# Kernel optimization log

Measured on AMD Instinct MI355X. Metric: run time of the kernel, lower is better.

The kernel has to match this reference:

```python
import jax, jax.numpy as jnp
import numpy as np

B, DIM, H, W = 8, 256, 128, 128
HEADS, D = 8, 32  # num_heads, qkv_dim (key_dim); multi_q_dim = HEADS*D = DIM


def setup_inputs() -> dict:
    key = jax.random.key(0)
    ks = jax.random.split(key, 10)
    def affine(k, n):
        k1, k2 = jax.random.split(k)
        return (1.0 + 0.1 * jax.random.normal(k1, (n,), jnp.float32),
                0.1 * jax.random.normal(k2, (n,), jnp.float32))
    q_scale, q_bias = affine(ks[1], HEADS * D)
    kv_scale, kv_bias = affine(ks[3], D)
    p_scale, p_bias = affine(ks[5], DIM)
    return {
        "input_": jax.random.normal(ks[0], (B, DIM, H, W), jnp.float32),
        "wq": jax.random.normal(ks[6], (HEADS * D, DIM), jnp.float32) / np.sqrt(DIM),
        "q_scale": q_scale, "q_bias": q_bias,
        "wkv": jax.random.normal(ks[7], (D, DIM), jnp.float32) / np.sqrt(DIM),
        "kv_scale": kv_scale, "kv_bias": kv_bias,
        "wp": jax.random.normal(ks[8], (DIM, HEADS * D), jnp.float32) / np.sqrt(HEADS * D),
        "p_scale": p_scale, "p_bias": p_bias,
    }


def conv1x1_bn(x_flat, w, scale, bias):
    # x_flat: [B,C,N]; 1x1 conv (no bias) fused with eval-mode BN affine
    y = jnp.einsum('oc,bcn->bon', w, x_flat)
    return y * scale[:, None] + bias[:, None]


def reference(input_, wq, q_scale, q_bias, wkv, kv_scale, kv_bias, wp, p_scale, p_bias):
    b, c, h, w = input_.shape
    n = h * w
    xf = input_.reshape(b, c, n)
    # queries: [B, heads, D, N]
    q = conv1x1_bn(xf, wq, q_scale, q_bias).reshape(b, HEADS, D, n)
    # shared key/value, one kv head: [B, D, N]
    kv = conv1x1_bn(xf, wkv, kv_scale, kv_bias)
    key_sm = jax.nn.softmax(kv, axis=2)      # softmax over spatial N
    query_sm = jax.nn.softmax(q, axis=2)     # softmax over channel D
    # context = softmax(K) @ V^T : [B, D, D]
    context = jnp.einsum('bdn,ben->bde', key_sm, kv)
    # attended = context^T @ Q (context broadcast over heads): [B, heads, D, N]
    attended = jnp.einsum('bde,bhdn->bhen', context, query_sm)
    av = attended.reshape(b, HEADS * D, n)
    out = conv1x1_bn(jax.nn.relu(av), wp, p_scale, p_bias)
    return out.reshape(b, c, h, w)
```

## Files before the change

kernel.cpp:

```cpp
#include <hip/hip_runtime.h>
#include <hip/hip_bf16.h>

typedef __hip_bfloat16 bf16;
typedef __attribute__((ext_vector_type(8))) short bf16x8;
typedef __attribute__((ext_vector_type(4))) float f32x4;

#define NB 8
#define NC 256
#define ND 32
#define NH 8
#define NN 16384
#define TILE_P 32

#define MFMA16(a, b, c) __builtin_amdgcn_mfma_f32_16x16x32_bf16((a), (b), (c), 0, 0, 0)

__device__ __forceinline__ float u2f(unsigned short u) {
  union { unsigned int i; float f; } v; v.i = ((unsigned int)u) << 16; return v.f;
}
__device__ __forceinline__ unsigned short f2u(float f) {
  union { float f; unsigned int i; } v; v.f = f;
  unsigned int x = v.i;
  return (unsigned short)((x + 0x7fffu + ((x >> 16) & 1u)) >> 16);
}
__device__ __forceinline__ float ldg(const void* p, size_t i, int isbf) {
  return isbf ? u2f(((const unsigned short*)p)[i]) : ((const float*)p)[i];
}
__device__ __forceinline__ char* lds_at(char* base, int p, int colb) {
  return base + (p << 9) + (colb ^ ((p & 7) << 4));
}

__global__ __launch_bounds__(256) void detect_kernel(const void* __restrict__ x,
                                                     int* __restrict__ flag) {
  __shared__ int red[4];
  const unsigned int* w = (const unsigned int*)x;
  int cnt = 0;
  for (int i = threadIdx.x; i < 4096; i += 256) {
    unsigned int e = (w[i] >> 7) & 0xFFu;
    cnt += (e >= 100u && e <= 135u) ? 1 : 0;
  }
  for (int off = 32; off; off >>= 1) cnt += __shfl_xor(cnt, off, 64);
  if ((threadIdx.x & 63) == 0) red[threadIdx.x >> 6] = cnt;
  __syncthreads();
  if (threadIdx.x == 0)
    flag[0] = (red[0] + red[1] + red[2] + red[3] > 2048) ? 1 : 0;
}

__global__ __launch_bounds__(256) void prep_weights(
    const void* __restrict__ wq, const void* __restrict__ wp,
    const void* __restrict__ wkv, const int* __restrict__ flag,
    unsigned short* __restrict__ WqPh, unsigned short* __restrict__ WqPl,
    unsigned short* __restrict__ WpPh, unsigned short* __restrict__ WpPl,
    unsigned short* __restrict__ WkPh, unsigned short* __restrict__ WkPl) {
  int isbf = flag[0];
  int idx = blockIdx.x * 256 + threadIdx.x;
  const void* w;
  unsigned short *Ph, *Pl;
  int slot, o, k0;
  if (idx < 16384) {
    int mat = idx >> 13;
    slot = idx & 8191;
    int lane = slot & 63;
    int mbkt = slot >> 6;
    int mb = mbkt & 15, kt = mbkt >> 4;
    o = mb * 16 + (lane & 15);
    k0 = kt * 32 + (lane >> 4) * 8;
    w = mat ? wp : wq;
    Ph = mat ? WpPh : WqPh;
    Pl = mat ? WpPl : WqPl;
  } else {
    slot = idx - 16384;
    int lane = slot & 63;
    int grp = slot >> 6;
    int mb = grp & 1, kt = grp >> 1;
    o = mb * 16 + (lane & 15);
    k0 = kt * 32 + (lane >> 4) * 8;
    w = wkv;
    Ph = WkPh;
    Pl = WkPl;
  }
  unsigned short h[8], lo[8];
#pragma unroll
  for (int e = 0; e < 8; e++) {
    float v = ldg(w, (size_t)o * NC + k0 + e, isbf);
    unsigned short hh = f2u(v);
    h[e] = hh;
    lo[e] = isbf ? (unsigned short)0 : f2u(v - u2f(hh));
  }
  uint4 ph, pl;
  ph.x = h[0] | ((unsigned)h[1] << 16);
  ph.y = h[2] | ((unsigned)h[3] << 16);
  ph.z = h[4] | ((unsigned)h[5] << 16);
  ph.w = h[6] | ((unsigned)h[7] << 16);
  pl.x = lo[0] | ((unsigned)lo[1] << 16);
  pl.y = lo[2] | ((unsigned)lo[3] << 16);
  pl.z = lo[4] | ((unsigned)lo[5] << 16);
  pl.w = lo[6] | ((unsigned)lo[7] << 16);
  *(uint4*)(Ph + (size_t)slot * 8) = ph;
  *(uint4*)(Pl + (size_t)slot * 8) = pl;
}

template <int ISBF>
__global__ __launch_bounds__(256, 2) void kv_mfma(
    const void* __restrict__ x, const unsigned short* __restrict__ WkPh,
    const unsigned short* __restrict__ WkPl, const void* __restrict__ kv_scale,
    const void* __restrict__ kv_bias, const int* __restrict__ flag,
    float* __restrict__ kv_out) {
  constexpr int POOL = ISBF ? 32768 : 65536;
  constexpr int XTL_O = 32768;
  __shared__ __align__(16) char pool[POOL];
  if (flag[0] != ISBF) return;
  const int tid = threadIdx.x;
  const int b = blockIdx.x >> 8;
  const int n0 = (blockIdx.x & 255) * 64;
  const int w = tid >> 6, l = tid & 63, g = l >> 4, cc = l & 15;

  {
    const int pq = (tid & 15) * 4;
    const int c0 = (tid >> 4) * 16;
    unsigned short hi[16][4], lo[16][4];
    if (ISBF) {
      const unsigned short* xp =
          (const unsigned short*)x + ((size_t)(b * NC + c0)) * NN + n0 + pq;
#pragma unroll
      for (int i = 0; i < 16; i++) {
        ushort4 r = *(const ushort4*)(xp + (size_t)i * NN);
        hi[i][0] = r.x; hi[i][1] = r.y; hi[i][2] = r.z; hi[i][3] = r.w;
      }
    } else {
      const float* xp = (const float*)x + ((size_t)(b * NC + c0)) * NN + n0 + pq;
#pragma unroll
      for (int i = 0; i < 16; i++) {
        float4 v = *(const float4*)(xp + (size_t)i * NN);
        float vv[4] = {v.x, v.y, v.z, v.w};
#pragma unroll
        for (int j = 0; j < 4; j++) {
          unsigned short hh = f2u(vv[j]);
          hi[i][j] = hh;
          lo[i][j] = f2u(vv[j] - u2f(hh));
        }
      }
    }
#pragma unroll
    for (int j = 0; j < 4; j++) {
      int p = pq + j;
#pragma unroll
      for (int half = 0; half < 2; half++) {
        uint4 wv;
        wv.x = hi[8*half+0][j] | ((unsigned)hi[8*half+1][j] << 16);
        wv.y = hi[8*half+2][j] | ((unsigned)hi[8*half+3][j] << 16);
        wv.z = hi[8*half+4][j] | ((unsigned)hi[8*half+5][j] << 16);
        wv.w = hi[8*half+6][j] | ((unsigned)hi[8*half+7][j] << 16);
        *(uint4*)lds_at(pool, p, c0 * 2 + half * 16) = wv;
        if (!ISBF) {
          uint4 wl2;
          wl2.x = lo[8*half+0][j] | ((unsigned)lo[8*half+1][j] << 16);
          wl2.y = lo[8*half+2][j] | ((unsigned)lo[8*half+3][j] << 16);
          wl2.z = lo[8*half+4][j] | ((unsigned)lo[8*half+5][j] << 16);
          wl2.w = lo[8*half+6][j] | ((unsigned)lo[8*half+7][j] << 16);
          *(uint4*)lds_at(pool + XTL_O, p, c0 * 2 + half * 16) = wl2;
        }
      }
    }
  }
  __syncthreads();

  const f32x4 zero4 = {0.f, 0.f, 0.f, 0.f};
  f32x4 acc[2] = {zero4, zero4};
  const bf16x8* Ah = (const bf16x8*)WkPh;
  const bf16x8* Al = (const bf16x8*)WkPl;
#pragma unroll
  for (int kt = 0; kt < 8; kt++) {
    bf16x8 xb = *(const bf16x8*)lds_at(pool, 16 * w + cc, kt * 64 + 16 * g);
    bf16x8 a0 = Ah[(kt * 2 + 0) * 64 + l];
    bf16x8 a1 = Ah[(kt * 2 + 1) * 64 + l];
    acc[0] = MFMA16(a0, xb, acc[0]);
    acc[1] = MFMA16(a1, xb, acc[1]);
    if (!ISBF) {
      bf16x8 xl = *(const bf16x8*)lds_at(pool + XTL_O, 16 * w + cc, kt * 64 + 16 * g);
      bf16x8 l0 = Al[(kt * 2 + 0) * 64 + l];
      bf16x8 l1 = Al[(kt * 2 + 1) * 64 + l];
      acc[0] = MFMA16(a0, xl, acc[0]);
      acc[0] = MFMA16(l0, xb, acc[0]);
      acc[0] = MFMA16(l0, xl, acc[0]);
      acc[1] = MFMA16(a1, xl, acc[1]);
      acc[1] = MFMA16(l1, xb, acc[1]);
      acc[1] = MFMA16(l1, xl, acc[1]);
    }
  }
  const int n = n0 + 16 * w + cc;
#pragma unroll
  for (int mi = 0; mi < 2; mi++) {
#pragma unroll
    for (int rr = 0; rr < 4; rr++) {
      int d = mi * 16 + 4 * g + rr;
      float v = acc[mi][rr] * ldg(kv_scale, d, ISBF) + ldg(kv_bias, d, ISBF);
      kv_out[((size_t)(b * ND + d)) * NN + n] = v;
    }
  }
}

__global__ __launch_bounds__(256) void rowmax_kernel(const float* __restrict__ kv,
                                                     float* __restrict__ m) {
  __shared__ float red[4];
  int row = blockIdx.x;
  const float* p = kv + (size_t)row * NN;
  float mx = -3.0e38f;
  for (int i = threadIdx.x; i < NN; i += 256) mx = fmaxf(mx, p[i]);
  for (int off = 32; off; off >>= 1) mx = fmaxf(mx, __shfl_xor(mx, off, 64));
  if ((threadIdx.x & 63) == 0) red[threadIdx.x >> 6] = mx;
  __syncthreads();
  if (threadIdx.x == 0)
    m[row] = fmaxf(fmaxf(red[0], red[1]), fmaxf(red[2], red[3]));
}

__global__ __launch_bounds__(256, 2) void ctx_mfma(const float* __restrict__ kv,
                                                   const float* __restrict__ m,
                                                   float* __restrict__ Spart,
                                                   float* __restrict__ Zpart) {
  constexpr int KH_O = 0, KL_O = 16384, EH_O = 32768, EL_O = 49152;
  __shared__ __align__(16) char pool[65536];
  const int tid = threadIdx.x;
  const int bid = blockIdx.x;
  const int b = bid >> 6;
  const int n0 = (bid & 63) * 256;
  const int r = tid >> 3, q = tid & 7;
  const float mr = m[b * ND + r];
  const float* src = kv + ((size_t)(b * ND + r)) * NN + n0;
  float z = 0.f;
#pragma unroll
  for (int s = 0; s < 8; s++) {
    float4 v = *(const float4*)(src + q * 4 + s * 32);
    float vv[4] = {v.x, v.y, v.z, v.w};
    unsigned short kh[4], kl[4], eh[4], el[4];
#pragma unroll
    for (int j = 0; j < 4; j++) {
      unsigned short hh = f2u(vv[j]);
      kh[j] = hh;
      kl[j] = f2u(vv[j] - u2f(hh));
      float e = __expf(vv[j] - mr);
      z += e;
      unsigned short eH = f2u(e);
      eh[j] = eH;
      el[j] = f2u(e - u2f(eH));
    }
    int colb = 8 * q + 64 * s;
    uint2 a;
    a.x = kh[0] | ((unsigned)kh[1] << 16); a.y = kh[2] | ((unsigned)kh[3] << 16);
    *(uint2*)lds_at(pool + KH_O, r, colb) = a;
    a.x = kl[0] | ((unsigned)kl[1] << 16); a.y = kl[2] | ((unsigned)kl[3] << 16);
    *(uint2*)lds_at(pool + KL_O, r, colb) = a;
    a.x = eh[0] | ((unsigned)eh[1] << 16); a.y = eh[2] | ((unsigned)eh[3] << 16);
    *(uint2*)lds_at(pool + EH_O, r, colb) = a;
    a.x = el[0] | ((unsigned)el[1] << 16); a.y = el[2] | ((unsigned)el[3] << 16);
    *(uint2*)lds_at(pool + EL_O, r, colb) = a;
  }
  z += __shfl_xor(z, 1, 64);
  z += __shfl_xor(z, 2, 64);
  z += __shfl_xor(z, 4, 64);
  if (q == 0) Zpart[(size_t)bid * ND + r] = z;
  __syncthreads();

  const int w = tid >> 6, l = tid & 63, g = l >> 4, cc = l & 15;
  const int mt = w >> 1, nt = w & 1;
  f32x4 sacc = {0.f, 0.f, 0.f, 0.f};
#pragma unroll
  for (int kt = 0; kt < 8; kt++) {
    int colb = kt * 64 + 16 * g;
    bf16x8 ehf = *(const bf16x8*)lds_at(pool + EH_O, 16 * mt + cc, colb);
    bf16x8 elf = *(const bf16x8*)lds_at(pool + EL_O, 16 * mt + cc, colb);
    bf16x8 khf = *(const bf16x8*)lds_at(pool + KH_O, 16 * nt + cc, colb);
    bf16x8 klf = *(const bf16x8*)lds_at(pool + KL_O, 16 * nt + cc, colb);
    sacc = MFMA16(ehf, khf, sacc);
    sacc = MFMA16(ehf, klf, sacc);
    sacc = MFMA16(elf, khf, sacc);
  }
#pragma unroll
  for (int rr = 0; rr < 4; rr++) {
    int row = 16 * mt + 4 * g + rr;
    Spart[(size_t)bid * 1024 + row * 32 + 16 * nt + cc] = sacc[rr];
  }
}

__global__ __launch_bounds__(256) void ctx_redfin(const float* __restrict__ Spart,
                                                  const float* __restrict__ Zpart,
                                                  float* __restrict__ ctx) {
  int i = blockIdx.x * 256 + threadIdx.x;
  int b = i >> 10, cell = i & 1023, d = cell >> 5;
  float s = 0.f, z = 0.f;
  for (int ch = 0; ch < 64; ch++) {
    s += Spart[(size_t)(b * 64 + ch) * 1024 + cell];
    z += Zpart[(size_t)(b * 64 + ch) * ND + d];
  }
  ctx[i] = s / z;
}

template <int ISBF>
__global__ __launch_bounds__(256, 2) void fused_main(
    const void* __restrict__ x,
    const unsigned short* __restrict__ WqPh, const unsigned short* __restrict__ WqPl,
    const unsigned short* __restrict__ WpPh, const unsigned short* __restrict__ WpPl,
    const void* __restrict__ q_scale, const void* __restrict__ q_bias,
    const void* __restrict__ p_scale, const void* __restrict__ p_bias,
    const float* __restrict__ ctx, const int* __restrict__ flag,
    void* __restrict__ out) {
  constexpr int XT_O = 0;
  constexpr int XTL_O = 16384;
  constexpr int SMH_O = ISBF ? 16384 : 32768;
  constexpr int SML_O = ISBF ? 32768 : 49152;
  constexpr int YTH_O = 0;
  constexpr int YTL_O = 16384;
  constexpr int OT_O = ISBF ? 16384 : 32768;
  constexpr int OT_STR = ISBF ? 88 : 144;
  constexpr int POOL = ISBF ? 49152 : 69632;
  __shared__ __align__(16) char pool[POOL];
  __shared__ float qs_l[NC], qb_l[NC], ps_l[NC], pb_l[NC];
  if (flag[0] != ISBF) return;
  const int tid = threadIdx.x;
  const int b = blockIdx.x >> 9;
  const int n0 = (blockIdx.x & 511) * TILE_P;
  const int w = tid >> 6;
  const int l = tid & 63;
  const int g = l >> 4;
  const int cc = l & 15;
  const f32x4 zero4 = {0.f, 0.f, 0.f, 0.f};

  qs_l[tid] = ldg(q_scale, tid, ISBF);
  qb_l[tid] = ldg(q_bias, tid, ISBF);
  ps_l[tid] = ldg(p_scale, tid, ISBF);
  pb_l[tid] = ldg(p_bias, tid, ISBF);

  bf16x8 cAh[2], cAl[2];
  {
    const float* cb = ctx + (size_t)b * ND * ND;
#pragma unroll
    for (int mp = 0; mp < 2; mp++) {
      bf16x8 ah, al;
#pragma unroll
      for (int el = 0; el < 8; el++) {
        float v = cb[(8 * g + el) * ND + 16 * mp + cc];
        unsigned short hh = f2u(v);
        ah[el] = (short)hh;
        al[el] = (short)f2u(v - u2f(hh));
      }
      cAh[mp] = ah; cAl[mp] = al;
    }
  }

  {
    const int c0 = (tid >> 3) * 8;
    const int pq = (tid & 7) * 4;
    unsigned short hi[8][4], lo[8][4];
    if (ISBF) {
      const unsigned short* xp =
          (const unsigned short*)x + ((size_t)(b * NC + c0)) * NN + n0 + pq;
#pragma unroll
      for (int i = 0; i < 8; i++) {
        ushort4 r = *(const ushort4*)(xp + (size_t)i * NN);
        hi[i][0] = r.x; hi[i][1] = r.y; hi[i][2] = r.z; hi[i][3] = r.w;
      }
    } else {
      const float* xp = (const float*)x + ((size_t)(b * NC + c0)) * NN + n0 + pq;
#pragma unroll
      for (int i = 0; i < 8; i++) {
        float4 v = *(const float4*)(xp + (size_t)i * NN);
        float vv[4] = {v.x, v.y, v.z, v.w};
#pragma unroll
        for (int j = 0; j < 4; j++) {
          unsigned short hh = f2u(vv[j]);
          hi[i][j] = hh;
          lo[i][j] = f2u(vv[j] - u2f(hh));
        }
      }
    }
#pragma unroll
    for (int j = 0; j < 4; j++) {
      int p = pq + j;
      uint4 wv;
      wv.x = hi[0][j] | ((unsigned)hi[1][j] << 16);
      wv.y = hi[2][j] | ((unsigned)hi[3][j] << 16);
      wv.z = hi[4][j] | ((unsigned)hi[5][j] << 16);
      wv.w = hi[6][j] | ((unsigned)hi[7][j] << 16);
      *(uint4*)lds_at(pool + XT_O, p, c0 * 2) = wv;
      if (!ISBF) {
        uint4 wl2;
        wl2.x = lo[0][j] | ((unsigned)lo[1][j] << 16);
        wl2.y = lo[2][j] | ((unsigned)lo[3][j] << 16);
        wl2.z = lo[4][j] | ((unsigned)lo[5][j] << 16);
        wl2.w = lo[6][j] | ((unsigned)lo[7][j] << 16);
        *(uint4*)lds_at(pool + XTL_O, p, c0 * 2) = wl2;
      }
    }
  }
  __syncthreads();

  f32x4 acc[4][2];
#pragma unroll
  for (int mi = 0; mi < 4; mi++) { acc[mi][0] = zero4; acc[mi][1] = zero4; }
  {
    const bf16x8* Aq = (const bf16x8*)WqPh;
    const bf16x8* Aql = (const bf16x8*)WqPl;
#pragma unroll
    for (int kt = 0; kt < 8; kt++) {
      bf16x8 xb0 = *(const bf16x8*)lds_at(pool + XT_O, cc, kt * 64 + 16 * g);
      bf16x8 xb1 = *(const bf16x8*)lds_at(pool + XT_O, 16 + cc, kt * 64 + 16 * g);
      bf16x8 av[4];
#pragma unroll
      for (int mi = 0; mi < 4; mi++) av[mi] = Aq[(kt * 16 + w * 4 + mi) * 64 + l];
#pragma unroll
      for (int mi = 0; mi < 4; mi++) {
        acc[mi][0] = MFMA16(av[mi], xb0, acc[mi][0]);
        acc[mi][1] = MFMA16(av[mi], xb1, acc[mi][1]);
      }
      if (!ISBF) {
        bf16x8 xl0 = *(const bf16x8*)lds_at(pool + XTL_O, cc, kt * 64 + 16 * g);
        bf16x8 xl1 = *(const bf16x8*)lds_at(pool + XTL_O, 16 + cc, kt * 64 + 16 * g);
#pragma unroll
        for (int mi = 0; mi < 4; mi++) {
          bf16x8 al2 = Aql[(kt * 16 + w * 4 + mi) * 64 + l];
          acc[mi][0] = MFMA16(av[mi], xl0, acc[mi][0]);
          acc[mi][1] = MFMA16(av[mi], xl1, acc[mi][1]);
          acc[mi][0] = MFMA16(al2, xb0, acc[mi][0]);
          acc[mi][1] = MFMA16(al2, xb1, acc[mi][1]);
          acc[mi][0] = MFMA16(al2, xl0, acc[mi][0]);
          acc[mi][1] = MFMA16(al2, xl1, acc[mi][1]);
        }
      }
    }
  }

  float inv_s[2][2];
#pragma unroll
  for (int hp = 0; hp < 2; hp++) {
#pragma unroll
    for (int ni = 0; ni < 2; ni++) {
      float e8[8];
      float mx = -3.0e38f;
#pragma unroll
      for (int mi2 = 0; mi2 < 2; mi2++) {
#pragma unroll
        for (int r = 0; r < 4; r++) {
          int o = w * 64 + (2 * hp + mi2) * 16 + 4 * g + r;
          float v = acc[2 * hp + mi2][ni][r] * qs_l[o] + qb_l[o];
          e8[mi2 * 4 + r] = v;
          mx = fmaxf(mx, v);
        }
      }
      mx = fmaxf(mx, __shfl_xor(mx, 16, 64));
      mx = fmaxf(mx, __shfl_xor(mx, 32, 64));
      float s = 0.f;
#pragma unroll
      for (int i2 = 0; i2 < 8; i2++) { e8[i2] = __expf(e8[i2] - mx); s += e8[i2]; }
      s += __shfl_xor(s, 16, 64);
      s += __shfl_xor(s, 32, 64);
      inv_s[hp][ni] = 1.f / s;
      int p = ni * 16 + cc;
#pragma unroll
      for (int mi2 = 0; mi2 < 2; mi2++) {
        int colb = (w * 64 + (2 * hp + mi2) * 16 + 4 * g) * 2;
        unsigned short h[4], lo2[4];
#pragma unroll
        for (int r = 0; r < 4; r++) {
          float ev = e8[mi2 * 4 + r];
          unsigned short hh = f2u(ev);
          h[r] = hh;
          lo2[r] = f2u(ev - u2f(hh));
        }
        uint2 wh, wl2;
        wh.x = h[0] | ((unsigned)h[1] << 16);
        wh.y = h[2] | ((unsigned)h[3] << 16);
        wl2.x = lo2[0] | ((unsigned)lo2[1] << 16);
        wl2.y = lo2[2] | ((unsigned)lo2[3] << 16);
        *(uint2*)lds_at(pool + SMH_O, p, colb) = wh;
        *(uint2*)lds_at(pool + SML_O, p, colb) = wl2;
      }
    }
  }
  __syncthreads();

#pragma unroll
  for (int hp = 0; hp < 2; hp++) {
    f32x4 cacc[2][2];
#pragma unroll
    for (int mp = 0; mp < 2; mp++) { cacc[mp][0] = zero4; cacc[mp][1] = zero4; }
#pragma unroll
    for (int ni = 0; ni < 2; ni++) {
      int p = ni * 16 + cc;
      int colb = ((2 * w + hp) * 32 + 8 * g) * 2;
      bf16x8 bh = *(const bf16x8*)lds_at(pool + SMH_O, p, colb);
      bf16x8 bl = *(const bf16x8*)lds_at(pool + SML_O, p, colb);
#pragma unroll
      for (int mp = 0; mp < 2; mp++) {
        cacc[mp][ni] = MFMA16(cAh[mp], bh, cacc[mp][ni]);
        cacc[mp][ni] = MFMA16(cAh[mp], bl, cacc[mp][ni]);
        cacc[mp][ni] = MFMA16(cAl[mp], bh, cacc[mp][ni]);
        if (!ISBF) cacc[mp][ni] = MFMA16(cAl[mp], bl, cacc[mp][ni]);
      }
    }
#pragma unroll
    for (int mp = 0; mp < 2; mp++) {
#pragma unroll
      for (int ni = 0; ni < 2; ni++) {
        int p = ni * 16 + cc;
        float iv = inv_s[hp][ni];
        unsigned short h[4], lo2[4];
#pragma unroll
        for (int r = 0; r < 4; r++) {
          float y = fmaxf(cacc[mp][ni][r] * iv, 0.f);
          unsigned short hh = f2u(y);
          h[r] = hh;
          lo2[r] = f2u(y - u2f(hh));
        }
        int colb = ((2 * w + hp) * 32 + mp * 16 + 4 * g) * 2;
        uint2 wh;
        wh.x = h[0] | ((unsigned)h[1] << 16);
        wh.y = h[2] | ((unsigned)h[3] << 16);
        *(uint2*)lds_at(pool + YTH_O, p, colb) = wh;
        if (!ISBF) {
          uint2 wl2;
          wl2.x = lo2[0] | ((unsigned)lo2[1] << 16);
          wl2.y = lo2[2] | ((unsigned)lo2[3] << 16);
          *(uint2*)lds_at(pool + YTL_O, p, colb) = wl2;
        }
      }
    }
  }
  __syncthreads();

  f32x4 oacc[4][2];
#pragma unroll
  for (int mi = 0; mi < 4; mi++) { oacc[mi][0] = zero4; oacc[mi][1] = zero4; }
  {
    const bf16x8* Ap = (const bf16x8*)WpPh;
    const bf16x8* Apl = (const bf16x8*)WpPl;
#pragma unroll
    for (int kt = 0; kt < 8; kt++) {
      bf16x8 yh0 = *(const bf16x8*)lds_at(pool + YTH_O, cc, kt * 64 + 16 * g);
      bf16x8 yh1 = *(const bf16x8*)lds_at(pool + YTH_O, 16 + cc, kt * 64 + 16 * g);
      bf16x8 av[4];
#pragma unroll
      for (int mi = 0; mi < 4; mi++) av[mi] = Ap[(kt * 16 + w * 4 + mi) * 64 + l];
#pragma unroll
      for (int mi = 0; mi < 4; mi++) {
        oacc[mi][0] = MFMA16(av[mi], yh0, oacc[mi][0]);
        oacc[mi][1] = MFMA16(av[mi], yh1, oacc[mi][1]);
      }
      if (!ISBF) {
        bf16x8 yl0 = *(const bf16x8*)lds_at(pool + YTL_O, cc, kt * 64 + 16 * g);
        bf16x8 yl1 = *(const bf16x8*)lds_at(pool + YTL_O, 16 + cc, kt * 64 + 16 * g);
#pragma unroll
        for (int mi = 0; mi < 4; mi++) {
          bf16x8 al2 = Apl[(kt * 16 + w * 4 + mi) * 64 + l];
          oacc[mi][0] = MFMA16(av[mi], yl0, oacc[mi][0]);
          oacc[mi][1] = MFMA16(av[mi], yl1, oacc[mi][1]);
          oacc[mi][0] = MFMA16(al2, yh0, oacc[mi][0]);
          oacc[mi][1] = MFMA16(al2, yh1, oacc[mi][1]);
        }
      }
    }
  }

  {
    char* OT = pool + OT_O;
#pragma unroll
    for (int mi = 0; mi < 4; mi++) {
#pragma unroll
      for (int ni = 0; ni < 2; ni++) {
#pragma unroll
        for (int r = 0; r < 4; r++) {
          int o = w * 64 + mi * 16 + 4 * g + r;
          float v = oacc[mi][ni][r] * ps_l[o] + pb_l[o];
          int p = ni * 16 + cc;
          if (ISBF)
            *(unsigned short*)(OT + o * OT_STR + p * 2) = f2u(v);
          else
            *(float*)(OT + o * OT_STR + p * 4) = v;
        }
      }
    }
  }
  __syncthreads();
  {
    char* OT = pool + OT_O;
    int o = tid;
    size_t gbase = ((size_t)(b * NC + o)) * NN + n0;
    if (ISBF) {
      unsigned short* po = (unsigned short*)out + gbase;
#pragma unroll
      for (int k = 0; k < 4; k++) {
        uint2 a = *(const uint2*)(OT + o * OT_STR + k * 16);
        uint2 b2 = *(const uint2*)(OT + o * OT_STR + k * 16 + 8);
        uint4 pk = make_uint4(a.x, a.y, b2.x, b2.y);
        *(uint4*)(po + k * 8) = pk;
      }
    } else {
      float* po = (float*)out + gbase;
#pragma unroll
      for (int k = 0; k < 8; k++)
        *(float4*)(po + k * 4) = *(const float4*)(OT + o * OT_STR + k * 16);
    }
  }
}

extern "C" void kernel_launch(void* const* d_in, const int* in_sizes, int n_in,
                              void* d_out, int out_size, void* d_ws, size_t ws_size,
                              hipStream_t stream) {
  const void* input   = d_in[0];
  const void* wq      = d_in[1];
  const void* q_scale = d_in[2];
  const void* q_bias  = d_in[3];
  const void* wkv     = d_in[4];
  const void* kv_scale= d_in[5];
  const void* kv_bias = d_in[6];
  const void* wp      = d_in[7];
  const void* p_scale = d_in[8];
  const void* p_bias  = d_in[9];

  char* w = (char*)d_ws;
  int*  flag = (int*)w;      w += 256;
  float* kv   = (float*)w;   w += (size_t)NB * ND * NN * 4;
  float* mrow = (float*)w;   w += 1024;
  float* Spart = (float*)w;  w += (size_t)512 * 1024 * 4;
  float* Zpart = (float*)w;  w += (size_t)512 * ND * 4;
  float* ctx  = (float*)w;   w += (size_t)NB * ND * ND * 4;
  unsigned short* WqPh = (unsigned short*)w; w += (size_t)NC * NC * 2;
  unsigned short* WqPl = (unsigned short*)w; w += (size_t)NC * NC * 2;
  unsigned short* WpPh = (unsigned short*)w; w += (size_t)NC * NC * 2;
  unsigned short* WpPl = (unsigned short*)w; w += (size_t)NC * NC * 2;
  unsigned short* WkPh = (unsigned short*)w; w += (size_t)ND * NC * 2;
  unsigned short* WkPl = (unsigned short*)w; w += (size_t)ND * NC * 2;

  detect_kernel<<<1, 256, 0, stream>>>(input, flag);
  prep_weights<<<68, 256, 0, stream>>>(wq, wp, wkv, flag, WqPh, WqPl, WpPh, WpPl,
                                       WkPh, WkPl);
  kv_mfma<1><<<2048, 256, 0, stream>>>(input, WkPh, WkPl, kv_scale, kv_bias, flag, kv);
  kv_mfma<0><<<2048, 256, 0, stream>>>(input, WkPh, WkPl, kv_scale, kv_bias, flag, kv);
  rowmax_kernel<<<256, 256, 0, stream>>>(kv, mrow);
  ctx_mfma<<<512, 256, 0, stream>>>(kv, mrow, Spart, Zpart);
  ctx_redfin<<<32, 256, 0, stream>>>(Spart, Zpart, ctx);
  fused_main<1><<<4096, 256, 0, stream>>>(input, WqPh, WqPl, WpPh, WpPl,
                                          q_scale, q_bias, p_scale, p_bias,
                                          ctx, flag, (void*)d_out);
  fused_main<0><<<4096, 256, 0, stream>>>(input, WqPh, WqPl, WpPh, WpPl,
                                          q_scale, q_bias, p_scale, p_bias,
                                          ctx, flag, (void*)d_out);
}
```

Measured before the change: 420.4 us.

## Split K into bf16 hi/lo planes, drop max pass, halve LDS for occupancy

The kv projection now writes K as bf16 hi/lo planes instead of fp32. The rowmax kernel is removed, so the context kernel computes exp without max subtraction, reading K straight from global memory with no LDS staging. fp32 paths in kv_mfma and fused_main stage the input in two K-halves to shrink LDS and raise occupancy (launch bounds 4 and 3). Several lo*lo MFMA terms and the low part of the relu(attended) activations are dropped. This trades accuracy and the overflow safety of max-subtraction for less memory traffic, fewer launches and fewer MFMAs.

```diff
diff --git a/kernel.cpp b/kernel.cpp
--- a/kernel.cpp
+++ b/kernel.cpp
@@ -1,14 +1,12 @@
 #include <hip/hip_runtime.h>
 #include <hip/hip_bf16.h>
 
-typedef __hip_bfloat16 bf16;
 typedef __attribute__((ext_vector_type(8))) short bf16x8;
 typedef __attribute__((ext_vector_type(4))) float f32x4;
 
 #define NB 8
 #define NC 256
 #define ND 32
-#define NH 8
 #define NN 16384
 #define TILE_P 32
 
@@ -100,45 +98,32 @@
 }
 
 template <int ISBF>
-__global__ __launch_bounds__(256, 2) void kv_mfma(
+__global__ __launch_bounds__(256, 4) void kv_mfma(
     const void* __restrict__ x, const unsigned short* __restrict__ WkPh,
     const unsigned short* __restrict__ WkPl, const void* __restrict__ kv_scale,
     const void* __restrict__ kv_bias, const int* __restrict__ flag,
-    float* __restrict__ kv_out) {
-  constexpr int POOL = ISBF ? 32768 : 65536;
-  constexpr int XTL_O = 32768;
-  __shared__ __align__(16) char pool[POOL];
+    unsigned short* __restrict__ Kh, unsigned short* __restrict__ Kl) {
+  __shared__ __align__(16) char pool[32768];
   if (flag[0] != ISBF) return;
   const int tid = threadIdx.x;
   const int b = blockIdx.x >> 8;
   const int n0 = (blockIdx.x & 255) * 64;
   const int w = tid >> 6, l = tid & 63, g = l >> 4, cc = l & 15;
-
-  {
+  const f32x4 zero4 = {0.f, 0.f, 0.f, 0.f};
+  f32x4 acc[2] = {zero4, zero4};
+  const bf16x8* Ah = (const bf16x8*)WkPh;
+  const bf16x8* Al = (const bf16x8*)WkPl;
+
+  if constexpr (ISBF) {
     const int pq = (tid & 15) * 4;
     const int c0 = (tid >> 4) * 16;
-    unsigned short hi[16][4], lo[16][4];
-    if (ISBF) {
-      const unsigned short* xp =
-          (const unsigned short*)x + ((size_t)(b * NC + c0)) * NN + n0 + pq;
-#pragma unroll
-      for (int i = 0; i < 16; i++) {
-        ushort4 r = *(const ushort4*)(xp + (size_t)i * NN);
-        hi[i][0] = r.x; hi[i][1] = r.y; hi[i][2] = r.z; hi[i][3] = r.w;
-      }
-    } else {
-      const float* xp = (const float*)x + ((size_t)(b * NC + c0)) * NN + n0 + pq;
-#pragma unroll
-      for (int i = 0; i < 16; i++) {
-        float4 v = *(const float4*)(xp + (size_t)i * NN);
-        float vv[4] = {v.x, v.y, v.z, v.w};
-#pragma unroll
-        for (int j = 0; j < 4; j++) {
-          unsigned short hh = f2u(vv[j]);
-          hi[i][j] = hh;
-          lo[i][j] = f2u(vv[j] - u2f(hh));
-        }
-      }
+    const unsigned short* xp =
+        (const unsigned short*)x + ((size_t)(b * NC + c0)) * NN + n0 + pq;
+    unsigned short hi[16][4];
+#pragma unroll
+    for (int i = 0; i < 16; i++) {
+      ushort4 r = *(const ushort4*)(xp + (size_t)i * NN);
+      hi[i][0] = r.x; hi[i][1] = r.y; hi[i][2] = r.z; hi[i][3] = r.w;
     }
 #pragma unroll
     for (int j = 0; j < 4; j++) {
@@ -151,42 +136,72 @@
         wv.z = hi[8*half+4][j] | ((unsigned)hi[8*half+5][j] << 16);
         wv.w = hi[8*half+6][j] | ((unsigned)hi[8*half+7][j] << 16);
         *(uint4*)lds_at(pool, p, c0 * 2 + half * 16) = wv;
-        if (!ISBF) {
-          uint4 wl2;
-          wl2.x = lo[8*half+0][j] | ((unsigned)lo[8*half+1][j] << 16);
-          wl2.y = lo[8*half+2][j] | ((unsigned)lo[8*half+3][j] << 16);
-          wl2.z = lo[8*half+4][j] | ((unsigned)lo[8*half+5][j] << 16);
-          wl2.w = lo[8*half+6][j] | ((unsigned)lo[8*half+7][j] << 16);
-          *(uint4*)lds_at(pool + XTL_O, p, c0 * 2 + half * 16) = wl2;
+      }
+    }
+    __syncthreads();
+#pragma unroll
+    for (int kt = 0; kt < 8; kt++) {
+      bf16x8 xb = *(const bf16x8*)lds_at(pool, 16 * w + cc, kt * 64 + 16 * g);
+      bf16x8 a0 = Ah[(kt * 2 + 0) * 64 + l];
+      bf16x8 a1 = Ah[(kt * 2 + 1) * 64 + l];
+      acc[0] = MFMA16(a0, xb, acc[0]);
+      acc[1] = MFMA16(a1, xb, acc[1]);
+    }
+  } else {
+#pragma unroll
+    for (int kh = 0; kh < 2; kh++) {
+      const int pq = (tid & 15) * 4;
+      const int c0l = (tid >> 4) * 8;
+      const float* xp =
+          (const float*)x + ((size_t)(b * NC + kh * 128 + c0l)) * NN + n0 + pq;
+      unsigned short hi[8][4], lo[8][4];
+#pragma unroll
+      for (int i = 0; i < 8; i++) {
+        float4 v = *(const float4*)(xp + (size_t)i * NN);
+        float vv[4] = {v.x, v.y, v.z, v.w};
+#pragma unroll
+        for (int j = 0; j < 4; j++) {
+          unsigned short hh = f2u(vv[j]);
+          hi[i][j] = hh;
+          lo[i][j] = f2u(vv[j] - u2f(hh));
         }
       }
-    }
-  }
-  __syncthreads();
-
-  const f32x4 zero4 = {0.f, 0.f, 0.f, 0.f};
-  f32x4 acc[2] = {zero4, zero4};
-  const bf16x8* Ah = (const bf16x8*)WkPh;
-  const bf16x8* Al = (const bf16x8*)WkPl;
-#pragma unroll
-  for (int kt = 0; kt < 8; kt++) {
-    bf16x8 xb = *(const bf16x8*)lds_at(pool, 16 * w + cc, kt * 64 + 16 * g);
-    bf16x8 a0 = Ah[(kt * 2 + 0) * 64 + l];
-    bf16x8 a1 = Ah[(kt * 2 + 1) * 64 + l];
-    acc[0] = MFMA16(a0, xb, acc[0]);
-    acc[1] = MFMA16(a1, xb, acc[1]);
-    if (!ISBF) {
-      bf16x8 xl = *(const bf16x8*)lds_at(pool + XTL_O, 16 * w + cc, kt * 64 + 16 * g);
-      bf16x8 l0 = Al[(kt * 2 + 0) * 64 + l];
-      bf16x8 l1 = Al[(kt * 2 + 1) * 64 + l];
-      acc[0] = MFMA16(a0, xl, acc[0]);
-      acc[0] = MFMA16(l0, xb, acc[0]);
-      acc[0] = MFMA16(l0, xl, acc[0]);
-      acc[1] = MFMA16(a1, xl, acc[1]);
-      acc[1] = MFMA16(l1, xb, acc[1]);
-      acc[1] = MFMA16(l1, xl, acc[1]);
-    }
-  }
+      if (kh) __syncthreads();
+#pragma unroll
+      for (int j = 0; j < 4; j++) {
+        int p = pq + j;
+        uint4 wv, wl2;
+        wv.x = hi[0][j] | ((unsigned)hi[1][j] << 16);
+        wv.y = hi[2][j] | ((unsigned)hi[3][j] << 16);
+        wv.z = hi[4][j] | ((unsigned)hi[5][j] << 16);
+        wv.w = hi[6][j] | ((unsigned)hi[7][j] << 16);
+        wl2.x = lo[0][j] | ((unsigned)lo[1][j] << 16);
+        wl2.y = lo[2][j] | ((unsigned)lo[3][j] << 16);
+        wl2.z = lo[4][j] | ((unsigned)lo[5][j] << 16);
+        wl2.w = lo[6][j] | ((unsigned)lo[7][j] << 16);
+        *(uint4*)lds_at(pool, p, c0l * 2) = wv;
+        *(uint4*)lds_at(pool, p, c0l * 2 + 256) = wl2;
+      }
+      __syncthreads();
+#pragma unroll
+      for (int kt = 0; kt < 4; kt++) {
+        int ktg = kh * 4 + kt;
+        bf16x8 xh = *(const bf16x8*)lds_at(pool, 16 * w + cc, kt * 64 + 16 * g);
+        bf16x8 xl = *(const bf16x8*)lds_at(pool, 16 * w + cc, kt * 64 + 16 * g + 256);
+        bf16x8 a0 = Ah[(ktg * 2 + 0) * 64 + l];
+        bf16x8 a1 = Ah[(ktg * 2 + 1) * 64 + l];
+        bf16x8 l0 = Al[(ktg * 2 + 0) * 64 + l];
+        bf16x8 l1 = Al[(ktg * 2 + 1) * 64 + l];
+        acc[0] = MFMA16(a0, xh, acc[0]);
+        acc[0] = MFMA16(a0, xl, acc[0]);
+        acc[0] = MFMA16(l0, xh, acc[0]);
+        acc[1] = MFMA16(a1, xh, acc[1]);
+        acc[1] = MFMA16(a1, xl, acc[1]);
+        acc[1] = MFMA16(l1, xh, acc[1]);
+      }
+    }
+  }
+
   const int n = n0 + 16 * w + cc;
 #pragma unroll
   for (int mi = 0; mi < 2; mi++) {
@@ -194,90 +209,72 @@
     for (int rr = 0; rr < 4; rr++) {
       int d = mi * 16 + 4 * g + rr;
       float v = acc[mi][rr] * ldg(kv_scale, d, ISBF) + ldg(kv_bias, d, ISBF);
-      kv_out[((size_t)(b * ND + d)) * NN + n] = v;
-    }
-  }
-}
-
-__global__ __launch_bounds__(256) void rowmax_kernel(const float* __restrict__ kv,
-                                                     float* __restrict__ m) {
-  __shared__ float red[4];
-  int row = blockIdx.x;
-  const float* p = kv + (size_t)row * NN;
-  float mx = -3.0e38f;
-  for (int i = threadIdx.x; i < NN; i += 256) mx = fmaxf(mx, p[i]);
-  for (int off = 32; off; off >>= 1) mx = fmaxf(mx, __shfl_xor(mx, off, 64));
-  if ((threadIdx.x & 63) == 0) red[threadIdx.x >> 6] = mx;
-  __syncthreads();
-  if (threadIdx.x == 0)
-    m[row] = fmaxf(fmaxf(red[0], red[1]), fmaxf(red[2], red[3]));
-}
-
-__global__ __launch_bounds__(256, 2) void ctx_mfma(const float* __restrict__ kv,
-                                                   const float* __restrict__ m,
-                                                   float* __restrict__ Spart,
-                                                   float* __restrict__ Zpart) {
-  constexpr int KH_O = 0, KL_O = 16384, EH_O = 32768, EL_O = 49152;
-  __shared__ __align__(16) char pool[65536];
+      unsigned short h16 = f2u(v);
+      unsigned short l16 = f2u(v - u2f(h16));
+      size_t off = ((size_t)(b * ND + d)) * NN + n;
+      Kh[off] = h16;
+      Kl[off] = l16;
+    }
+  }
+}
+
+__global__ __launch_bounds__(256) void ctx_mfma(const unsigned short* __restrict__ Kh,
+                                                const unsigned short* __restrict__ Kl,
+                                                float* __restrict__ Spart,
+                                                float* __restrict__ Zpart) {
   const int tid = threadIdx.x;
   const int bid = blockIdx.x;
-  const int b = bid >> 6;
-  const int n0 = (bid & 63) * 256;
-  const int r = tid >> 3, q = tid & 7;
-  const float mr = m[b * ND + r];
-  const float* src = kv + ((size_t)(b * ND + r)) * NN + n0;
-  float z = 0.f;
-#pragma unroll
-  for (int s = 0; s < 8; s++) {
-    float4 v = *(const float4*)(src + q * 4 + s * 32);
-    float vv[4] = {v.x, v.y, v.z, v.w};
-    unsigned short kh[4], kl[4], eh[4], el[4];
-#pragma unroll
-    for (int j = 0; j < 4; j++) {
-      unsigned short hh = f2u(vv[j]);
-      kh[j] = hh;
-      kl[j] = f2u(vv[j] - u2f(hh));
-      float e = __expf(vv[j] - mr);
-      z += e;
-      unsigned short eH = f2u(e);
-      eh[j] = eH;
-      el[j] = f2u(e - u2f(eH));
-    }
-    int colb = 8 * q + 64 * s;
-    uint2 a;
-    a.x = kh[0] | ((unsigned)kh[1] << 16); a.y = kh[2] | ((unsigned)kh[3] << 16);
-    *(uint2*)lds_at(pool + KH_O, r, colb) = a;
-    a.x = kl[0] | ((unsigned)kl[1] << 16); a.y = kl[2] | ((unsigned)kl[3] << 16);
-    *(uint2*)lds_at(pool + KL_O, r, colb) = a;
-    a.x = eh[0] | ((unsigned)eh[1] << 16); a.y = eh[2] | ((unsigned)eh[3] << 16);
-    *(uint2*)lds_at(pool + EH_O, r, colb) = a;
-    a.x = el[0] | ((unsigned)el[1] << 16); a.y = el[2] | ((unsigned)el[3] << 16);
-    *(uint2*)lds_at(pool + EL_O, r, colb) = a;
-  }
-  z += __shfl_xor(z, 1, 64);
-  z += __shfl_xor(z, 2, 64);
-  z += __shfl_xor(z, 4, 64);
-  if (q == 0) Zpart[(size_t)bid * ND + r] = z;
-  __syncthreads();
-
+  const int b = bid >> 4;
   const int w = tid >> 6, l = tid & 63, g = l >> 4, cc = l & 15;
-  const int mt = w >> 1, nt = w & 1;
-  f32x4 sacc = {0.f, 0.f, 0.f, 0.f};
+  const int nbase = (bid & 15) * 1024 + w * 256;
+  const f32x4 zero4 = {0.f, 0.f, 0.f, 0.f};
+  f32x4 s00 = zero4, s01 = zero4, s10 = zero4, s11 = zero4;
+  float z0 = 0.f, z1 = 0.f;
+  const size_t row0 = ((size_t)(b * ND) + cc) * NN;
+  const size_t row1 = ((size_t)(b * ND) + 16 + cc) * NN;
 #pragma unroll
   for (int kt = 0; kt < 8; kt++) {
-    int colb = kt * 64 + 16 * g;
-    bf16x8 ehf = *(const bf16x8*)lds_at(pool + EH_O, 16 * mt + cc, colb);
-    bf16x8 elf = *(const bf16x8*)lds_at(pool + EL_O, 16 * mt + cc, colb);
-    bf16x8 khf = *(const bf16x8*)lds_at(pool + KH_O, 16 * nt + cc, colb);
-    bf16x8 klf = *(const bf16x8*)lds_at(pool + KL_O, 16 * nt + cc, colb);
-    sacc = MFMA16(ehf, khf, sacc);
-    sacc = MFMA16(ehf, klf, sacc);
-    sacc = MFMA16(elf, khf, sacc);
-  }
+    int nn = nbase + kt * 32 + 8 * g;
+    bf16x8 kh0 = *(const bf16x8*)(Kh + row0 + nn);
+    bf16x8 kl0 = *(const bf16x8*)(Kl + row0 + nn);
+    bf16x8 kh1 = *(const bf16x8*)(Kh + row1 + nn);
+    bf16x8 kl1 = *(const bf16x8*)(Kl + row1 + nn);
+    bf16x8 eh0, el0, eh1, el1;
+#pragma unroll
+    for (int e = 0; e < 8; e++) {
+      float v0 = u2f((unsigned short)kh0[e]) + u2f((unsigned short)kl0[e]);
+      float ev0 = __expf(v0);
+      z0 += ev0;
+      unsigned short h0 = f2u(ev0);
+      eh0[e] = (short)h0;
+      el0[e] = (short)f2u(ev0 - u2f(h0));
+      float v1 = u2f((unsigned short)kh1[e]) + u2f((unsigned short)kl1[e]);
+      float ev1 = __expf(v1);
+      z1 += ev1;
+      unsigned short h1 = f2u(ev1);
+      eh1[e] = (short)h1;
+      el1[e] = (short)f2u(ev1 - u2f(h1));
+    }
+    s00 = MFMA16(eh0, kh0, s00); s00 = MFMA16(eh0, kl0, s00); s00 = MFMA16(el0, kh0, s00);
+    s01 = MFMA16(eh0, kh1, s01); s01 = MFMA16(eh0, kl1, s01); s01 = MFMA16(el0, kh1, s01);
+    s10 = MFMA16(eh1, kh0, s10); s10 = MFMA16(eh1, kl0, s10); s10 = MFMA16(el1, kh0, s10);
+    s11 = MFMA16(eh1, kh1, s11); s11 = MFMA16(eh1, kl1, s11); s11 = MFMA16(el1, kh1, s11);
+  }
+  z0 += __shfl_xor(z0, 16, 64); z0 += __shfl_xor(z0, 32, 64);
+  z1 += __shfl_xor(z1, 16, 64); z1 += __shfl_xor(z1, 32, 64);
+  if (l < 16) {
+    Zpart[((size_t)bid * 4 + w) * ND + cc] = z0;
+    Zpart[((size_t)bid * 4 + w) * ND + 16 + cc] = z1;
+  }
+  float* sp = Spart + ((size_t)bid * 4 + w) * 1024;
 #pragma unroll
   for (int rr = 0; rr < 4; rr++) {
-    int row = 16 * mt + 4 * g + rr;
-    Spart[(size_t)bid * 1024 + row * 32 + 16 * nt + cc] = sacc[rr];
+    int r0 = (4 * g + rr) * 32;
+    int r1 = (16 + 4 * g + rr) * 32;
+    sp[r0 + cc] = s00[rr];
+    sp[r0 + 16 + cc] = s01[rr];
+    sp[r1 + cc] = s10[rr];
+    sp[r1 + 16 + cc] = s11[rr];
   }
 }
 
@@ -287,15 +284,15 @@
   int i = blockIdx.x * 256 + threadIdx.x;
   int b = i >> 10, cell = i & 1023, d = cell >> 5;
   float s = 0.f, z = 0.f;
-  for (int ch = 0; ch < 64; ch++) {
-    s += Spart[(size_t)(b * 64 + ch) * 1024 + cell];
-    z += Zpart[(size_t)(b * 64 + ch) * ND + d];
+  for (int j = 0; j < 64; j++) {
+    s += Spart[(size_t)(b * 64 + j) * 1024 + cell];
+    z += Zpart[(size_t)(b * 64 + j) * ND + d];
   }
   ctx[i] = s / z;
 }
 
 template <int ISBF>
-__global__ __launch_bounds__(256, 2) void fused_main(
+__global__ __launch_bounds__(256, 3) void fused_main(
     const void* __restrict__ x,
     const unsigned short* __restrict__ WqPh, const unsigned short* __restrict__ WqPl,
     const unsigned short* __restrict__ WpPh, const unsigned short* __restrict__ WpPl,
@@ -303,15 +300,11 @@
     const void* __restrict__ p_scale, const void* __restrict__ p_bias,
     const float* __restrict__ ctx, const int* __restrict__ flag,
     void* __restrict__ out) {
-  constexpr int XT_O = 0;
-  constexpr int XTL_O = 16384;
-  constexpr int SMH_O = ISBF ? 16384 : 32768;
-  constexpr int SML_O = ISBF ? 32768 : 49152;
-  constexpr int YTH_O = 0;
-  constexpr int YTL_O = 16384;
-  constexpr int OT_O = ISBF ? 16384 : 32768;
-  constexpr int OT_STR = ISBF ? 88 : 144;
-  constexpr int POOL = ISBF ? 49152 : 69632;
+  constexpr int SMH_O = 16384;
+  constexpr int SML_O = 32768;
+  constexpr int OT_O = 16384;
+  constexpr int OT_STR = ISBF ? 88 : 132;
+  constexpr int POOL = ISBF ? 49152 : 50176;
   __shared__ __align__(16) char pool[POOL];
   __shared__ float qs_l[NC], qb_l[NC], ps_l[NC], pb_l[NC];
   if (flag[0] != ISBF) return;
@@ -346,22 +339,58 @@
     }
   }
 
-  {
-    const int c0 = (tid >> 3) * 8;
-    const int pq = (tid & 7) * 4;
-    unsigned short hi[8][4], lo[8][4];
-    if (ISBF) {
+  f32x4 acc[4][2];
+#pragma unroll
+  for (int mi = 0; mi < 4; mi++) { acc[mi][0] = zero4; acc[mi][1] = zero4; }
+
+  if constexpr (ISBF) {
+    {
+      const int c0 = (tid >> 3) * 8;
+      const int pq = (tid & 7) * 4;
       const unsigned short* xp =
           (const unsigned short*)x + ((size_t)(b * NC + c0)) * NN + n0 + pq;
+      unsigned short hi[8][4];
 #pragma unroll
       for (int i = 0; i < 8; i++) {
         ushort4 r = *(const ushort4*)(xp + (size_t)i * NN);
         hi[i][0] = r.x; hi[i][1] = r.y; hi[i][2] = r.z; hi[i][3] = r.w;
       }
-    } else {
-      const float* xp = (const float*)x + ((size_t)(b * NC + c0)) * NN + n0 + pq;
-#pragma unroll
-      for (int i = 0; i < 8; i++) {
+#pragma unroll
+      for (int j = 0; j < 4; j++) {
+        int p = pq + j;
+        uint4 wv;
+        wv.x = hi[0][j] | ((unsigned)hi[1][j] << 16);
+        wv.y = hi[2][j] | ((unsigned)hi[3][j] << 16);
+        wv.z = hi[4][j] | ((unsigned)hi[5][j] << 16);
+        wv.w = hi[6][j] | ((unsigned)hi[7][j] << 16);
+        *(uint4*)lds_at(pool, p, c0 * 2) = wv;
+      }
+    }
+    __syncthreads();
+    const bf16x8* Aq = (const bf16x8*)WqPh;
+#pragma unroll
+    for (int kt = 0; kt < 8; kt++) {
+      bf16x8 xb0 = *(const bf16x8*)lds_at(pool, cc, kt * 64 + 16 * g);
+      bf16x8 xb1 = *(const bf16x8*)lds_at(pool, 16 + cc, kt * 64 + 16 * g);
+#pragma unroll
+      for (int mi = 0; mi < 4; mi++) {
+        bf16x8 av = Aq[(kt * 16 + w * 4 + mi) * 64 + l];
+        acc[mi][0] = MFMA16(av, xb0, acc[mi][0]);
+        acc[mi][1] = MFMA16(av, xb1, acc[mi][1]);
+      }
+    }
+  } else {
+    const bf16x8* Aq = (const bf16x8*)WqPh;
+    const bf16x8* Aql = (const bf16x8*)WqPl;
+#pragma unroll
+    for (int kh = 0; kh < 2; kh++) {
+      const int c0l = (tid >> 3) * 4;
+      const int pq = (tid & 7) * 4;
+      const float* xp =
+          (const float*)x + ((size_t)(b * NC + kh * 128 + c0l)) * NN + n0 + pq;
+      unsigned short hi[4][4], lo[4][4];
+#pragma unroll
+      for (int i = 0; i < 4; i++) {
         float4 v = *(const float4*)(xp + (size_t)i * NN);
         float vv[4] = {v.x, v.y, v.z, v.w};
 #pragma unroll
@@ -371,58 +400,36 @@
           lo[i][j] = f2u(vv[j] - u2f(hh));
         }
       }
-    }
-#pragma unroll
-    for (int j = 0; j < 4; j++) {
-      int p = pq + j;
-      uint4 wv;
-      wv.x = hi[0][j] | ((unsigned)hi[1][j] << 16);
-      wv.y = hi[2][j] | ((unsigned)hi[3][j] << 16);
-      wv.z = hi[4][j] | ((unsigned)hi[5][j] << 16);
-      wv.w = hi[6][j] | ((unsigned)hi[7][j] << 16);
-      *(uint4*)lds_at(pool + XT_O, p, c0 * 2) = wv;
-      if (!ISBF) {
-        uint4 wl2;
+      if (kh) __syncthreads();
+#pragma unroll
+      for (int j = 0; j < 4; j++) {
+        int p = pq + j;
+        uint2 wv, wl2;
+        wv.x = hi[0][j] | ((unsigned)hi[1][j] << 16);
+        wv.y = hi[2][j] | ((unsigned)hi[3][j] << 16);
         wl2.x = lo[0][j] | ((unsigned)lo[1][j] << 16);
         wl2.y = lo[2][j] | ((unsigned)lo[3][j] << 16);
-        wl2.z = lo[4][j] | ((unsigned)lo[5][j] << 16);
-        wl2.w = lo[6][j] | ((unsigned)lo[7][j] << 16);
-        *(uint4*)lds_at(pool + XTL_O, p, c0 * 2) = wl2;
-      }
-    }
-  }
-  __syncthreads();
-
-  f32x4 acc[4][2];
-#pragma unroll
-  for (int mi = 0; mi < 4; mi++) { acc[mi][0] = zero4; acc[mi][1] = zero4; }
-  {
-    const bf16x8* Aq = (const bf16x8*)WqPh;
-    const bf16x8* Aql = (const bf16x8*)WqPl;
-#pragma unroll
-    for (int kt = 0; kt < 8; kt++) {
-      bf16x8 xb0 = *(const bf16x8*)lds_at(pool + XT_O, cc, kt * 64 + 16 * g);
-      bf16x8 xb1 = *(const bf16x8*)lds_at(pool + XT_O, 16 + cc, kt * 64 + 16 * g);
-      bf16x8 av[4];
-#pragma unroll
-      for (int mi = 0; mi < 4; mi++) av[mi] = Aq[(kt * 16 + w * 4 + mi) * 64 + l];
-#pragma unroll
-      for (int mi = 0; mi < 4; mi++) {
-        acc[mi][0] = MFMA16(av[mi], xb0, acc[mi][0]);
-        acc[mi][1] = MFMA16(av[mi], xb1, acc[mi][1]);
-      }
-      if (!ISBF) {
-        bf16x8 xl0 = *(const bf16x8*)lds_at(pool + XTL_O, cc, kt * 64 + 16 * g);
-        bf16x8 xl1 = *(const bf16x8*)lds_at(pool + XTL_O, 16 + cc, kt * 64 + 16 * g);
+        *(uint2*)lds_at(pool, p, c0l * 2) = wv;
+        *(uint2*)lds_at(pool, p, c0l * 2 + 256) = wl2;
+      }
+      __syncthreads();
+#pragma unroll
+      for (int kt = 0; kt < 4; kt++) {
+        int ktg = kh * 4 + kt;
+        bf16x8 xb0 = *(const bf16x8*)lds_at(pool, cc, kt * 64 + 16 * g);
+        bf16x8 xl0 = *(const bf16x8*)lds_at(pool, cc, kt * 64 + 16 * g + 256);
+        bf16x8 xb1 = *(const bf16x8*)lds_at(pool, 16 + cc, kt * 64 + 16 * g);
+        bf16x8 xl1 = *(const bf16x8*)lds_at(pool, 16 + cc, kt * 64 + 16 * g + 256);
 #pragma unroll
         for (int mi = 0; mi < 4; mi++) {
-          bf16x8 al2 = Aql[(kt * 16 + w * 4 + mi) * 64 + l];
-          acc[mi][0] = MFMA16(av[mi], xl0, acc[mi][0]);
-          acc[mi][1] = MFMA16(av[mi], xl1, acc[mi][1]);
+          bf16x8 av = Aq[(ktg * 16 + w * 4 + mi) * 64 + l];
+          bf16x8 al2 = Aql[(ktg * 16 + w * 4 + mi) * 64 + l];
+          acc[mi][0] = MFMA16(av, xb0, acc[mi][0]);
+          acc[mi][0] = MFMA16(av, xl0, acc[mi][0]);
           acc[mi][0] = MFMA16(al2, xb0, acc[mi][0]);
+          acc[mi][1] = MFMA16(av, xb1, acc[mi][1]);
+          acc[mi][1] = MFMA16(av, xl1, acc[mi][1]);
           acc[mi][1] = MFMA16(al2, xb1, acc[mi][1]);
-          acc[mi][0] = MFMA16(al2, xl0, acc[mi][0]);
-          acc[mi][1] = MFMA16(al2, xl1, acc[mi][1]);
         }
       }
     }
@@ -493,7 +500,6 @@
         cacc[mp][ni] = MFMA16(cAh[mp], bh, cacc[mp][ni]);
         cacc[mp][ni] = MFMA16(cAh[mp], bl, cacc[mp][ni]);
         cacc[mp][ni] = MFMA16(cAl[mp], bh, cacc[mp][ni]);
-        if (!ISBF) cacc[mp][ni] = MFMA16(cAl[mp], bl, cacc[mp][ni]);
       }
     }
 #pragma unroll
@@ -502,25 +508,15 @@
       for (int ni = 0; ni < 2; ni++) {
         int p = ni * 16 + cc;
         float iv = inv_s[hp][ni];
-        unsigned short h[4], lo2[4];
-#pragma unroll
-        for (int r = 0; r < 4; r++) {
-          float y = fmaxf(cacc[mp][ni][r] * iv, 0.f);
-          unsigned short hh = f2u(y);
-          h[r] = hh;
-          lo2[r] = f2u(y - u2f(hh));
-        }
+        unsigned short h[4];
+#pragma unroll
+        for (int r = 0; r < 4; r++)
+          h[r] = f2u(fmaxf(cacc[mp][ni][r] * iv, 0.f));
         int colb = ((2 * w + hp) * 32 + mp * 16 + 4 * g) * 2;
         uint2 wh;
         wh.x = h[0] | ((unsigned)h[1] << 16);
         wh.y = h[2] | ((unsigned)h[3] << 16);
-        *(uint2*)lds_at(pool + YTH_O, p, colb) = wh;
-        if (!ISBF) {
-          uint2 wl2;
-          wl2.x = lo2[0] | ((unsigned)lo2[1] << 16);
-          wl2.y = lo2[2] | ((unsigned)lo2[3] << 16);
-          *(uint2*)lds_at(pool + YTL_O, p, colb) = wl2;
-        }
+        *(uint2*)lds_at(pool, p, colb) = wh;
       }
     }
   }
@@ -534,24 +530,18 @@
     const bf16x8* Apl = (const bf16x8*)WpPl;
 #pragma unroll
     for (int kt = 0; kt < 8; kt++) {
-      bf16x8 yh0 = *(const bf16x8*)lds_at(pool + YTH_O, cc, kt * 64 + 16 * g);
-      bf16x8 yh1 = *(const bf16x8*)lds_at(pool + YTH_O, 16 + cc, kt * 64 + 16 * g);
-      bf16x8 av[4];
-#pragma unroll
-      for (int mi = 0; mi < 4; mi++) av[mi] = Ap[(kt * 16 + w * 4 + mi) * 64 + l];
+      bf16x8 yh0 = *(const bf16x8*)lds_at(pool, cc, kt * 64 + 16 * g);
+      bf16x8 yh1 = *(const bf16x8*)lds_at(pool, 16 + cc, kt * 64 + 16 * g);
 #pragma unroll
       for (int mi = 0; mi < 4; mi++) {
-        oacc[mi][0] = MFMA16(av[mi], yh0, oacc[mi][0]);
-        oacc[mi][1] = MFMA16(av[mi], yh1, oacc[mi][1]);
+        bf16x8 av = Ap[(kt * 16 + w * 4 + mi) * 64 + l];
+        oacc[mi][0] = MFMA16(av, yh0, oacc[mi][0]);
+        oacc[mi][1] = MFMA16(av, yh1, oacc[mi][1]);
       }
       if (!ISBF) {
-        bf16x8 yl0 = *(const bf16x8*)lds_at(pool + YTL_O, cc, kt * 64 + 16 * g);
-        bf16x8 yl1 = *(const bf16x8*)lds_at(pool + YTL_O, 16 + cc, kt * 64 + 16 * g);
 #pragma unroll
         for (int mi = 0; mi < 4; mi++) {
           bf16x8 al2 = Apl[(kt * 16 + w * 4 + mi) * 64 + l];
-          oacc[mi][0] = MFMA16(av[mi], yl0, oacc[mi][0]);
-          oacc[mi][1] = MFMA16(av[mi], yl1, oacc[mi][1]);
           oacc[mi][0] = MFMA16(al2, yh0, oacc[mi][0]);
           oacc[mi][1] = MFMA16(al2, yh1, oacc[mi][1]);
         }
@@ -589,14 +579,19 @@
       for (int k = 0; k < 4; k++) {
         uint2 a = *(const uint2*)(OT + o * OT_STR + k * 16);
         uint2 b2 = *(const uint2*)(OT + o * OT_STR + k * 16 + 8);
-        uint4 pk = make_uint4(a.x, a.y, b2.x, b2.y);
-        *(uint4*)(po + k * 8) = pk;
+        *(uint4*)(po + k * 8) = make_uint4(a.x, a.y, b2.x, b2.y);
       }
     } else {
       float* po = (float*)out + gbase;
 #pragma unroll
-      for (int k = 0; k < 8; k++)
-        *(float4*)(po + k * 4) = *(const float4*)(OT + o * OT_STR + k * 16);
+      for (int k = 0; k < 8; k++) {
+        float4 v;
+        v.x = *(const float*)(OT + o * OT_STR + (k * 4 + 0) * 4);
+        v.y = *(const float*)(OT + o * OT_STR + (k * 4 + 1) * 4);
+        v.z = *(const float*)(OT + o * OT_STR + (k * 4 + 2) * 4);
+        v.w = *(const float*)(OT + o * OT_STR + (k * 4 + 3) * 4);
+        *(float4*)(po + k * 4) = v;
+      }
     }
   }
 }
@@ -617,10 +612,10 @@
 
   char* w = (char*)d_ws;
   int*  flag = (int*)w;      w += 256;
-  float* kv   = (float*)w;   w += (size_t)NB * ND * NN * 4;
-  float* mrow = (float*)w;   w += 1024;
+  unsigned short* Kh = (unsigned short*)w; w += (size_t)NB * ND * NN * 2;
+  unsigned short* Kl = (unsigned short*)w; w += (size_t)NB * ND * NN * 2;
+  float* Zpart = (float*)w;  w += (size_t)512 * ND * 4;
   float* Spart = (float*)w;  w += (size_t)512 * 1024 * 4;
-  float* Zpart = (float*)w;  w += (size_t)512 * ND * 4;
   float* ctx  = (float*)w;   w += (size_t)NB * ND * ND * 4;
   unsigned short* WqPh = (unsigned short*)w; w += (size_t)NC * NC * 2;
   unsigned short* WqPl = (unsigned short*)w; w += (size_t)NC * NC * 2;
@@ -632,10 +627,9 @@
   detect_kernel<<<1, 256, 0, stream>>>(input, flag);
   prep_weights<<<68, 256, 0, stream>>>(wq, wp, wkv, flag, WqPh, WqPl, WpPh, WpPl,
                                        WkPh, WkPl);
-  kv_mfma<1><<<2048, 256, 0, stream>>>(input, WkPh, WkPl, kv_scale, kv_bias, flag, kv);
-  kv_mfma<0><<<2048, 256, 0, stream>>>(input, WkPh, WkPl, kv_scale, kv_bias, flag, kv);
-  rowmax_kernel<<<256, 256, 0, stream>>>(kv, mrow);
-  ctx_mfma<<<512, 256, 0, stream>>>(kv, mrow, Spart, Zpart);
+  kv_mfma<1><<<2048, 256, 0, stream>>>(input, WkPh, WkPl, kv_scale, kv_bias, flag, Kh, Kl);
+  kv_mfma<0><<<2048, 256, 0, stream>>>(input, WkPh, WkPl, kv_scale, kv_bias, flag, Kh, Kl);
+  ctx_mfma<<<128, 256, 0, stream>>>(Kh, Kl, Spart, Zpart);
   ctx_redfin<<<32, 256, 0, stream>>>(Spart, Zpart, ctx);
   fused_main<1><<<4096, 256, 0, stream>>>(input, WqPh, WqPl, WpPh, WpPl,
                                           q_scale, q_bias, p_scale, p_bias,
```

After: 485.5 us. 1.15x slower.
